# Optimization experiments

Hardware: AMD Instinct MI355X
Metric: run time of the kernel (lower is better)

## Reference

```python
import jax, jax.numpy as jnp
import numpy as np

BATCH = 128
SITES = 256      # input_dim, number of MPS input cores
BOND = 64        # bond dimension D
FEAT = 2         # feature_dim
OUT = 10         # output_dim


def setup_inputs() -> dict:
    key = jax.random.key(0)
    k1, k2, k3, k4, k5 = jax.random.split(key, 5)
    # forward input: [batch, input_dim, feature_dim], values in [0,1) like a feature map
    input_data = jax.random.uniform(k1, (BATCH, SITES, FEAT), dtype=jnp.float32)
    # InputRegion core tensor, bond_str 'slri' -> [sites, D, D, feat]
    # small random perturbation; identity bias (use_bias=True, fixed_bias) added in forward
    cores = 0.01 * jax.random.normal(k2, (SITES, BOND, BOND, FEAT), dtype=jnp.float32)
    # OutputSite core, bond_str 'olr' -> [output_dim, D, D]
    out_core = 0.01 * jax.random.normal(k3, (OUT, BOND, BOND), dtype=jnp.float32)
    # boundary (edge) vectors for open boundary conditions
    left_vec = jax.random.normal(k4, (BOND,), dtype=jnp.float32) / np.sqrt(BOND)
    right_vec = jax.random.normal(k5, (BOND,), dtype=jnp.float32) / np.sqrt(BOND)
    return {"input_data": input_data, "cores": cores, "out_core": out_core,
            "left_vec": left_vec, "right_vec": right_vec}


def _chain_matmul(mats):
    """Log-depth product of a chain of matrices. mats: [b, s, D, D] -> [b, D, D].
    Product is ordered: mats[:,0] @ mats[:,1] @ ... @ mats[:,s-1]."""
    b, s, d, _ = mats.shape
    while mats.shape[1] > 1:
        n = mats.shape[1]
        if n % 2 == 1:  # pad with identity so length is even
            eye = jnp.broadcast_to(jnp.eye(d, dtype=mats.dtype), (b, 1, d, d))
            mats = jnp.concatenate([mats, eye], axis=1)
        mats = jnp.matmul(mats[:, 0::2], mats[:, 1::2])
    return mats[:, 0]


def reference(input_data, cores, out_core, left_vec, right_vec):
    # InputRegion.forward: contract each core with its per-site feature vector
    # 'slri,bsi->bslr', then add identity bias matrix (use_bias=True)
    mats = jnp.einsum('slri,bsi->bslr', cores, input_data)
    mats = mats + jnp.eye(BOND, dtype=mats.dtype)  # bias_mat = eye, broadcast over b,s

    # split the chain around the (central) output site, reduce each side
    half = SITES // 2
    left_prod = _chain_matmul(mats[:, :half])    # [b, D, D]
    right_prod = _chain_matmul(mats[:, half:])   # [b, D, D]

    # open-boundary contraction: lvec . Lprod . out_core . Rprod . rvec -> [b, out]
    v = jnp.einsum('l,blr->br', left_vec, left_prod)        # [b, D]
    v = jnp.einsum('bl,olr->bor', v, out_core)              # [b, out, D]
    v = jnp.einsum('bol,blr->bor', v, right_prod)           # [b, out, D]
    logits = jnp.einsum('bor,r->bo', v, right_vec)          # [b, out]
    return logits
```

## Files before the change

kernel.cpp:

```cpp
#include <hip/hip_runtime.h>

#define BOND   64
#define SITES  256
#define HALF   128
#define NBATCH 128
#define OUTD   10

#define P1_OFF   1048576
#define VEC_OFF  2097152
#define SITE_F4  2048
#define LPITCH   132

__global__ void __launch_bounds__(256)
mps_pack_kernel(const float* __restrict__ cores, float* __restrict__ P) {
  __shared__ __align__(16) float ld[64 * LPITCH];
  const int s = (int)blockIdx.x;
  const int t = (int)threadIdx.x;
  const float4* src = (const float4*)(cores + (size_t)s * 8192);
  #pragma unroll
  for (int k = 0; k < 8; ++k) {
    const int m = t + 256 * k;
    const int row = m >> 5;
    const int c4  = m & 31;
    *(float4*)&ld[row * LPITCH + c4 * 4] = src[m];
  }
  __syncthreads();
  const bool right = s >= HALF;
  const int step = right ? (SITES - 1 - s) : s;
  float4* out = (float4*)(P + (right ? P1_OFF : 0)) + (size_t)step * SITE_F4;
  #pragma unroll
  for (int k = 0; k < 8; ++k) {
    const int m = t + 256 * k;
    const int g = m >> 6;
    const int j = m & 63;
    float4 v;
    if (!right) {
      const float2 a  = *(const float2*)&ld[(2 * g) * LPITCH + 2 * j];
      const float2 b2 = *(const float2*)&ld[(2 * g + 1) * LPITCH + 2 * j];
      v = make_float4(a.x, a.y, b2.x, b2.y);
    } else {
      v = *(const float4*)&ld[j * LPITCH + 4 * g];
    }
    out[m] = v;
  }
}

__device__ __forceinline__ float rlanef(float v, int l) {
  return __int_as_float(__builtin_amdgcn_readlane(__float_as_int(v), l));
}

__global__ void __launch_bounds__(256, 1)
mps_chain_kernel(const float* __restrict__ input,
                 const float* __restrict__ P,
                 const float* __restrict__ lvec,
                 const float* __restrict__ rvec,
                 float* __restrict__ vout) {
  __shared__ __align__(16) float pa0[2][4][BOND];
  __shared__ __align__(16) float pa1[2][4][BOND];
  __shared__ __align__(16) float xsh[2][HALF][2];

  const int t    = (int)threadIdx.x;
  const int w    = t >> 6;
  const int lane = t & 63;
  const int side = (int)blockIdx.x & 1;
  const int pair = (int)blockIdx.x >> 1;
  const int b0   = 2 * pair;
  const int b1   = 2 * pair + 1;

  {
    const int bi = t >> 7;
    const int st = t & 127;
    const int b  = bi ? b1 : b0;
    const int hs = side ? (HALF - 1 - st) : st;
    const float2 xv =
        *(const float2*)(input + ((size_t)b * SITES + side * HALF + hs) * 2);
    xsh[bi][st][0] = xv.x;
    xsh[bi][st][1] = xv.y;
  }

  const float e = side ? rvec[lane] : lvec[lane];
  float r0 = e, r1 = e;

  const int wb = 16 * w;
  float u0[16], u1[16];
  #pragma unroll
  for (int k = 0; k < 16; ++k) {
    u0[k] = rlanef(r0, wb + k);
    u1[k] = rlanef(r1, wb + k);
  }

  const float4* base = (const float4*)(P + (side ? P1_OFF : 0)) +
                       (size_t)(8 * w) * 64 + lane;

  float4 A[8], B[8];
  #pragma unroll
  for (int j = 0; j < 8; ++j) A[j] = base[j * 64];

  __syncthreads();

  #define STEP(CUR, NXT, I)                                                  \
  {                                                                          \
    const int inx = ((I) + 1 < HALF) ? (I) + 1 : (I);                        \
    _Pragma("unroll")                                                        \
    for (int j = 0; j < 8; ++j) NXT[j] = base[(size_t)inx * 2048 + j * 64];  \
    float p00 = 0.f, p01 = 0.f, p10 = 0.f, p11 = 0.f;                        \
    _Pragma("unroll")                                                        \
    for (int g = 0; g < 8; ++g) {                                            \
      const float4 m = CUR[g];                                               \
      p00 = __builtin_fmaf(u0[2 * g], m.x, p00);                             \
      p01 = __builtin_fmaf(u0[2 * g], m.y, p01);                             \
      p10 = __builtin_fmaf(u1[2 * g], m.x, p10);                             \
      p11 = __builtin_fmaf(u1[2 * g], m.y, p11);                             \
      p00 = __builtin_fmaf(u0[2 * g + 1], m.z, p00);                         \
      p01 = __builtin_fmaf(u0[2 * g + 1], m.w, p01);                         \
      p10 = __builtin_fmaf(u1[2 * g + 1], m.z, p10);                         \
      p11 = __builtin_fmaf(u1[2 * g + 1], m.w, p11);                         \
    }                                                                        \
    const float2 x0 = *(const float2*)xsh[0][(I)];                           \
    const float2 x1 = *(const float2*)xsh[1][(I)];                           \
    const float t0 = __builtin_fmaf(x0.x, p00, x0.y * p01);                  \
    const float t1 = __builtin_fmaf(x1.x, p10, x1.y * p11);                  \
    pa0[(I) & 1][w][lane] = t0;                                              \
    pa1[(I) & 1][w][lane] = t1;                                              \
    asm volatile("s_waitcnt lgkmcnt(0)" ::: "memory");                       \
    __builtin_amdgcn_s_barrier();                                            \
    r0 += (pa0[(I) & 1][0][lane] + pa0[(I) & 1][1][lane]) +                  \
          (pa0[(I) & 1][2][lane] + pa0[(I) & 1][3][lane]);                   \
    r1 += (pa1[(I) & 1][0][lane] + pa1[(I) & 1][1][lane]) +                  \
          (pa1[(I) & 1][2][lane] + pa1[(I) & 1][3][lane]);                   \
    _Pragma("unroll")                                                        \
    for (int k = 0; k < 16; ++k) {                                           \
      u0[k] = rlanef(r0, wb + k);                                            \
      u1[k] = rlanef(r1, wb + k);                                            \
    }                                                                        \
  }

  for (int i = 0; i < HALF; i += 2) {
    STEP(A, B, i);
    STEP(B, A, i + 1);
  }
  #undef STEP

  if (w == 0) {
    vout[((size_t)side * NBATCH + b0) * BOND + lane] = r0;
    vout[((size_t)side * NBATCH + b1) * BOND + lane] = r1;
  }
}

__global__ void __launch_bounds__(64)
mps_combine_kernel(const float* __restrict__ oc,
                   const float* __restrict__ vecs,
                   float* __restrict__ out) {
  __shared__ float vl[BOND];
  const int lane = (int)threadIdx.x;
  const int b = (int)blockIdx.x;
  vl[lane] = vecs[b * BOND + lane];
  const float myvr = vecs[NBATCH * BOND + b * BOND + lane];
  float res[OUTD];
  #pragma unroll
  for (int o = 0; o < OUTD; ++o) {
    float acc = 0.f;
    #pragma unroll
    for (int m = 0; m < BOND; ++m)
      acc = __builtin_fmaf(vl[m], oc[((o * BOND) + m) * BOND + lane], acc);
    acc *= myvr;
    #pragma unroll
    for (int off = 32; off > 0; off >>= 1)
      acc += __shfl_xor(acc, off, 64);
    res[o] = acc;
  }
  if (lane == 0) {
    #pragma unroll
    for (int o = 0; o < OUTD; ++o) out[b * OUTD + o] = res[o];
  }
}

extern "C" void kernel_launch(void* const* d_in, const int* in_sizes, int n_in,
                              void* d_out, int out_size, void* d_ws, size_t ws_size,
                              hipStream_t stream) {
  const float* input = (const float*)d_in[0];
  const float* cores = (const float*)d_in[1];
  const float* oc    = (const float*)d_in[2];
  const float* lvec  = (const float*)d_in[3];
  const float* rvec  = (const float*)d_in[4];
  float* ws  = (float*)d_ws;
  float* out = (float*)d_out;

  hipLaunchKernelGGL(mps_pack_kernel, dim3(SITES), dim3(256), 0, stream,
                     cores, ws);
  hipLaunchKernelGGL(mps_chain_kernel, dim3(NBATCH), dim3(256), 0, stream,
                     input, ws, lvec, rvec, ws + VEC_OFF);
  hipLaunchKernelGGL(mps_combine_kernel, dim3(NBATCH), dim3(64), 0, stream,
                     oc, ws + VEC_OFF, out);
}
```

Baseline: 146.4 us.

## Assign one batch element per wavefront, removing per-step block barriers

The chain kernel used to split each step's 64-row vector-matrix product across four waves, for two batch elements, with a block barrier and an LDS reduction every step. Now each wavefront owns one batch element and does the full 64x64x2 contraction itself. It holds the whole site core in registers, double-buffered at 32 float4 per buffer, and shares its state vector through wave-private LDS. This removes the block-wide barrier and readlane broadcasts from the serial critical path. In exchange it needs very high VGPR use, multiplies redundant L2 reads of the cores, and halves the grid to 64 blocks.

Result: slower. 219.4 us (+49.9%).

```diff
diff --git a/kernel.cpp b/kernel.cpp
--- a/kernel.cpp
+++ b/kernel.cpp
@@ -45,94 +45,72 @@
   }
 }
 
-__device__ __forceinline__ float rlanef(float v, int l) {
-  return __int_as_float(__builtin_amdgcn_readlane(__float_as_int(v), l));
-}
-
 __global__ void __launch_bounds__(256, 1)
 mps_chain_kernel(const float* __restrict__ input,
                  const float* __restrict__ P,
                  const float* __restrict__ lvec,
                  const float* __restrict__ rvec,
                  float* __restrict__ vout) {
-  __shared__ __align__(16) float pa0[2][4][BOND];
-  __shared__ __align__(16) float pa1[2][4][BOND];
-  __shared__ __align__(16) float xsh[2][HALF][2];
+  __shared__ __align__(16) float vbuf[4][BOND];
+  __shared__ __align__(16) float xbuf[4][HALF][2];
 
   const int t    = (int)threadIdx.x;
   const int w    = t >> 6;
   const int lane = t & 63;
   const int side = (int)blockIdx.x & 1;
-  const int pair = (int)blockIdx.x >> 1;
-  const int b0   = 2 * pair;
-  const int b1   = 2 * pair + 1;
+  const int b    = ((int)blockIdx.x >> 1) * 4 + w;
 
+  float* xw = &xbuf[w][0][0];
   {
-    const int bi = t >> 7;
-    const int st = t & 127;
-    const int b  = bi ? b1 : b0;
-    const int hs = side ? (HALF - 1 - st) : st;
-    const float2 xv =
-        *(const float2*)(input + ((size_t)b * SITES + side * HALF + hs) * 2);
-    xsh[bi][st][0] = xv.x;
-    xsh[bi][st][1] = xv.y;
+    const float4 g =
+        ((const float4*)(input + (size_t)b * SITES * 2 + side * HALF * 2))[lane];
+    if (!side) {
+      ((float4*)xw)[lane] = g;
+    } else {
+      ((float2*)xw)[HALF - 1 - 2 * lane] = make_float2(g.x, g.y);
+      ((float2*)xw)[HALF - 2 - 2 * lane] = make_float2(g.z, g.w);
+    }
   }
 
-  const float e = side ? rvec[lane] : lvec[lane];
-  float r0 = e, r1 = e;
+  float r = side ? rvec[lane] : lvec[lane];
+  vbuf[w][lane] = r;
 
-  const int wb = 16 * w;
-  float u0[16], u1[16];
+  const float4* base = (const float4*)(P + (side ? P1_OFF : 0)) + lane;
+
+  float4 A[32], B[32];
   #pragma unroll
-  for (int k = 0; k < 16; ++k) {
-    u0[k] = rlanef(r0, wb + k);
-    u1[k] = rlanef(r1, wb + k);
-  }
-
-  const float4* base = (const float4*)(P + (side ? P1_OFF : 0)) +
-                       (size_t)(8 * w) * 64 + lane;
-
-  float4 A[8], B[8];
-  #pragma unroll
-  for (int j = 0; j < 8; ++j) A[j] = base[j * 64];
-
-  __syncthreads();
+  for (int j = 0; j < 32; ++j) A[j] = base[j * 64];
 
   #define STEP(CUR, NXT, I)                                                  \
   {                                                                          \
+                                       \
+    float4 vv[16];                                                           \
+    _Pragma("unroll")                                                        \
+    for (int k = 0; k < 16; ++k) vv[k] = ((const float4*)vbuf[w])[k];        \
+    const float2 xv = *(const float2*)&xw[2 * (I)];                          \
+              \
     const int inx = ((I) + 1 < HALF) ? (I) + 1 : (I);                        \
     _Pragma("unroll")                                                        \
-    for (int j = 0; j < 8; ++j) NXT[j] = base[(size_t)inx * 2048 + j * 64];  \
-    float p00 = 0.f, p01 = 0.f, p10 = 0.f, p11 = 0.f;                        \
+    for (int j = 0; j < 32; ++j)                                             \
+      NXT[j] = base[(size_t)inx * SITE_F4 + j * 64];                         \
+    asm volatile("" ::: "memory");                                           \
+    float p0a = 0.f, p1a = 0.f, p0b = 0.f, p1b = 0.f;                        \
     _Pragma("unroll")                                                        \
-    for (int g = 0; g < 8; ++g) {                                            \
-      const float4 m = CUR[g];                                               \
-      p00 = __builtin_fmaf(u0[2 * g], m.x, p00);                             \
-      p01 = __builtin_fmaf(u0[2 * g], m.y, p01);                             \
-      p10 = __builtin_fmaf(u1[2 * g], m.x, p10);                             \
-      p11 = __builtin_fmaf(u1[2 * g], m.y, p11);                             \
-      p00 = __builtin_fmaf(u0[2 * g + 1], m.z, p00);                         \
-      p01 = __builtin_fmaf(u0[2 * g + 1], m.w, p01);                         \
-      p10 = __builtin_fmaf(u1[2 * g + 1], m.z, p10);                         \
-      p11 = __builtin_fmaf(u1[2 * g + 1], m.w, p11);                         \
+    for (int q = 0; q < 16; ++q) {                                           \
+      const float4 vq = vv[q];                            \
+      const float4 m0 = CUR[2 * q];                       \
+      const float4 m1 = CUR[2 * q + 1];                   \
+      p0a = __builtin_fmaf(vq.x, m0.x, p0a);                                 \
+      p1a = __builtin_fmaf(vq.x, m0.y, p1a);                                 \
+      p0b = __builtin_fmaf(vq.z, m1.x, p0b);                                 \
+      p1b = __builtin_fmaf(vq.z, m1.y, p1b);                                 \
+      p0a = __builtin_fmaf(vq.y, m0.z, p0a);                                 \
+      p1a = __builtin_fmaf(vq.y, m0.w, p1a);                                 \
+      p0b = __builtin_fmaf(vq.w, m1.z, p0b);                                 \
+      p1b = __builtin_fmaf(vq.w, m1.w, p1b);                                 \
     }                                                                        \
-    const float2 x0 = *(const float2*)xsh[0][(I)];                           \
-    const float2 x1 = *(const float2*)xsh[1][(I)];                           \
-    const float t0 = __builtin_fmaf(x0.x, p00, x0.y * p01);                  \
-    const float t1 = __builtin_fmaf(x1.x, p10, x1.y * p11);                  \
-    pa0[(I) & 1][w][lane] = t0;                                              \
-    pa1[(I) & 1][w][lane] = t1;                                              \
-    asm volatile("s_waitcnt lgkmcnt(0)" ::: "memory");                       \
-    __builtin_amdgcn_s_barrier();                                            \
-    r0 += (pa0[(I) & 1][0][lane] + pa0[(I) & 1][1][lane]) +                  \
-          (pa0[(I) & 1][2][lane] + pa0[(I) & 1][3][lane]);                   \
-    r1 += (pa1[(I) & 1][0][lane] + pa1[(I) & 1][1][lane]) +                  \
-          (pa1[(I) & 1][2][lane] + pa1[(I) & 1][3][lane]);                   \
-    _Pragma("unroll")                                                        \
-    for (int k = 0; k < 16; ++k) {                                           \
-      u0[k] = rlanef(r0, wb + k);                                            \
-      u1[k] = rlanef(r1, wb + k);                                            \
-    }                                                                        \
+    r = __builtin_fmaf(xv.x, p0a + p0b, __builtin_fmaf(xv.y, p1a + p1b, r)); \
+    vbuf[w][lane] = r;                                                       \
   }
 
   for (int i = 0; i < HALF; i += 2) {
@@ -141,10 +119,7 @@
   }
   #undef STEP
 
-  if (w == 0) {
-    vout[((size_t)side * NBATCH + b0) * BOND + lane] = r0;
-    vout[((size_t)side * NBATCH + b1) * BOND + lane] = r1;
-  }
+  vout[((size_t)side * NBATCH + b) * BOND + lane] = r;
 }
 
 __global__ void __launch_bounds__(64)
@@ -188,7 +163,7 @@
 
   hipLaunchKernelGGL(mps_pack_kernel, dim3(SITES), dim3(256), 0, stream,
                      cores, ws);
-  hipLaunchKernelGGL(mps_chain_kernel, dim3(NBATCH), dim3(256), 0, stream,
+  hipLaunchKernelGGL(mps_chain_kernel, dim3(64), dim3(256), 0, stream,
                      input, ws, lvec, rvec, ws + VEC_OFF);
   hipLaunchKernelGGL(mps_combine_kernel, dim3(NBATCH), dim3(64), 0, stream,
                      oc, ws + VEC_OFF, out);
```
